# Kernel tuning notes

Hardware: AMD Instinct MI355X
Metric: run time of the kernel (lower is better)

Reference implementation:

```python
import jax, jax.numpy as jnp
import numpy as np

C = 128         # sphere_channels
H = 512         # hidden_channels
EC = 128        # edge_channels
LMAX = 4
K = 4           # num_experts
N_EQ = 2        # ceil(K/2) equivariant experts
N_NE = 2
N_NODES = 8192
N_EDGES = 262144
DEG_SIZES = np.array([2 * l + 1 for l in range(LMAX + 1)])  # [1,3,5,7,9]
M = int(DEG_SIZES.sum())  # 25 coeffs


def setup_inputs() -> dict:
    key = jax.random.key(0)
    ks = jax.random.split(key, 20)
    s = 0.02
    return {
        "x_emb": jax.random.normal(ks[0], (N_NODES, M, C), jnp.float32),
        "t_ij": jax.random.normal(ks[1], (N_EDGES, EC), jnp.float32),
        "edge_index": jax.random.randint(ks[2], (2, N_EDGES), 0, N_NODES, jnp.int32),
        # equivariant experts (stacked on leading expert axis)
        "eq_w1": jax.random.normal(ks[3], (N_EQ, C, H), jnp.float32) * s,
        "eq_gate_w": jax.random.normal(ks[4], (N_EQ, EC, H * (LMAX + 1)), jnp.float32) * s,
        "eq_gate_b": jax.random.normal(ks[5], (N_EQ, H * (LMAX + 1)), jnp.float32) * s,
        "eq_w2": jax.random.normal(ks[6], (N_EQ, H, C), jnp.float32) * s,
        # non-equivariant experts
        "ne_w1": jax.random.normal(ks[7], (N_NE, C, H), jnp.float32) * s,
        "ne_b1": jax.random.normal(ks[8], (N_NE, H), jnp.float32) * s,
        "ne_gate_w": jax.random.normal(ks[9], (N_NE, EC, H), jnp.float32) * s,
        "ne_gate_b": jax.random.normal(ks[10], (N_NE, H), jnp.float32) * s,
        "ne_w2": jax.random.normal(ks[11], (N_NE, H, C), jnp.float32) * s,
        "ne_b2": jax.random.normal(ks[12], (N_NE, C), jnp.float32) * s,
        # router
        "r_w1": jax.random.normal(ks[13], (EC, EC), jnp.float32) * s,
        "r_b1": jax.random.normal(ks[14], (EC,), jnp.float32) * s,
        "r_w2": jax.random.normal(ks[15], (EC, K), jnp.float32) * s,
        "r_b2": jax.random.normal(ks[16], (K,), jnp.float32) * s,
    }


def reference(x_emb, t_ij, edge_index, eq_w1, eq_gate_w, eq_gate_b, eq_w2,
              ne_w1, ne_b1, ne_gate_w, ne_gate_b, ne_w2, ne_b2,
              r_w1, r_b1, r_w2, r_b2):
    N = x_emb.shape[0]
    silu = jax.nn.silu

    # c_i = scatter-mean of t_ij onto destination nodes
    dst = edge_index[1]
    sums = jax.ops.segment_sum(t_ij, dst, num_segments=N)
    cnt = jax.ops.segment_sum(jnp.ones((t_ij.shape[0],), t_ij.dtype), dst, num_segments=N)
    c = sums / jnp.maximum(cnt, 1.0)[:, None]  # [N, EC]

    # soft routing weights from context
    w = jax.nn.softmax(silu(c @ r_w1 + r_b1) @ r_w2 + r_b2, axis=-1)  # [N, K]

    repeats = jnp.asarray(DEG_SIZES)
    is_scalar = (jnp.arange(M) == 0)[:, None]  # l=0 coeff mask, [M,1]

    # --- equivariant experts (vectorized over expert axis e) ---
    h = jnp.einsum('nmc,ech->enmh', x_emb, eq_w1)                      # [e,N,M,H]
    g = silu(jnp.einsum('nc,ecg->eng', c, eq_gate_w) + eq_gate_b[:, None, :])
    g = g.reshape(N_EQ, N, LMAX + 1, H)
    g = jnp.repeat(g, repeats, axis=2, total_repeat_length=M)          # [e,N,M,H]
    h = jnp.where(is_scalar, silu(h), h) * g                           # SiLU only on l=0
    out_eq = jnp.einsum('enmh,ehc->enmc', h, eq_w2)

    # --- non-equivariant experts ---
    h2 = silu(jnp.einsum('nmc,ech->enmh', x_emb, ne_w1) + ne_b1[:, None, None, :])
    g2 = silu(jnp.einsum('nc,ech->enh', c, ne_gate_w) + ne_gate_b[:, None, :])
    h2 = h2 * g2[:, :, None, :]
    out_ne = jnp.einsum('enmh,ehc->enmc', h2, ne_w2) + ne_b2[:, None, None, :]

    # softmax-weighted mixture (equiv experts first, matching ModuleList order)
    out = (jnp.einsum('nk,knmc->nmc', w[:, :N_EQ], out_eq)
           + jnp.einsum('nk,knmc->nmc', w[:, N_EQ:], out_ne))
    return out
```

## Files before the change

kernel.cpp:

```cpp
#include <hip/hip_runtime.h>

#define NNODES 8192
#define NEDGES 262144
#define CCH    128
#define HCH    512
#define GCOLS  6144
#define ROWS   204800
#define XSPAD  136
#define HGPAD  72

typedef __bf16 bf16_t;
typedef __bf16 bf16x8 __attribute__((ext_vector_type(8)));
typedef __bf16 bf16x4 __attribute__((ext_vector_type(4)));
typedef float  f32x4  __attribute__((ext_vector_type(4)));

__device__ __forceinline__ float siluf(float x) {
  return x * __builtin_amdgcn_rcpf(1.f + __expf(-x));
}

#define GLOAD_LDS(g, l) __builtin_amdgcn_global_load_lds( \
    (const __attribute__((address_space(1))) void*)(g), \
    (__attribute__((address_space(3))) void*)(l), 16, 0, 0)

constexpr size_t OFF_CSUM  = 0;
constexpr size_t OFF_DEG   = 4194304;
constexpr size_t OFF_OFFS  = 4227072;
constexpr size_t OFF_CUR   = 4263936;
constexpr size_t OFF_EIDS  = 4296704;
constexpr size_t OFF_WRT   = 5345280;
constexpr size_t OFF_CBF   = 5476352;
constexpr size_t OFF_WPT   = 7573504;
constexpr size_t OFF_BPK   = 9146368;
constexpr size_t OFF_W1T   = 9170944;
constexpr size_t OFF_W2T   = 9695232;
constexpr size_t OFF_GATES = 10219520;

__global__ __launch_bounds__(256) void edge_count_kernel(
    const int* __restrict__ edge_index, int* __restrict__ deg)
{
  int e = blockIdx.x * 256 + threadIdx.x;
  atomicAdd(&deg[edge_index[NEDGES + e]], 1);
}

__global__ __launch_bounds__(256) void scan_kernel(
    const int* __restrict__ deg, int* __restrict__ offs, int* __restrict__ cur)
{
  __shared__ int part[256];
  int t = threadIdx.x;
  int s = 0;
  #pragma unroll 4
  for (int i = 0; i < 32; ++i) s += deg[t * 32 + i];
  part[t] = s;
  __syncthreads();
  int incl = s;
  for (int off = 1; off < 256; off <<= 1) {
    int u = (t >= off) ? part[t - off] : 0;
    __syncthreads();
    incl += u;
    part[t] = incl;
    __syncthreads();
  }
  int run = incl - s;
  for (int i = 0; i < 32; ++i) {
    int d = deg[t * 32 + i];
    offs[t * 32 + i] = run;
    cur[t * 32 + i]  = run;
    run += d;
  }
  if (t == 255) offs[8192] = run;
}

__global__ __launch_bounds__(256) void edge_fill_kernel(
    const int* __restrict__ edge_index, int* __restrict__ cur, int* __restrict__ eids)
{
  int e = blockIdx.x * 256 + threadIdx.x;
  int dst = edge_index[NEDGES + e];
  int pos = atomicAdd(&cur[dst], 1);
  eids[pos] = e;
}

__global__ __launch_bounds__(128) void gather_mean_kernel(
    const float* __restrict__ t_ij, const int* __restrict__ offs,
    const int* __restrict__ eids, float* __restrict__ csum, bf16_t* __restrict__ cbf)
{
  int n = blockIdx.x, tid = threadIdx.x;
  int o0 = offs[n], o1 = offs[n + 1];
  float a0 = 0.f, a1 = 0.f;
  int j = o0;
  for (; j + 1 < o1; j += 2) {
    int e0 = eids[j], e1 = eids[j + 1];
    a0 += t_ij[(size_t)e0 * CCH + tid];
    a1 += t_ij[(size_t)e1 * CCH + tid];
  }
  if (j < o1) a0 += t_ij[(size_t)eids[j] * CCH + tid];
  float m = (a0 + a1) / fmaxf((float)(o1 - o0), 1.f);
  csum[(size_t)n * CCH + tid] = m;
  cbf[(size_t)n * CCH + tid]  = (bf16_t)m;
}

__global__ __launch_bounds__(256) void pack_kernel(
    const float* __restrict__ eq_gate_w, const float* __restrict__ ne_gate_w,
    const float* __restrict__ eq_gate_b, const float* __restrict__ ne_gate_b,
    const float* __restrict__ eq_w1, const float* __restrict__ ne_w1,
    const float* __restrict__ eq_w2, const float* __restrict__ ne_w2,
    bf16_t* __restrict__ WpackT, float* __restrict__ bpack,
    bf16_t* __restrict__ w1T, bf16_t* __restrict__ w2c)
{
  int idx = blockIdx.x * 256 + threadIdx.x;
  if (idx < 786432) {
    int j = idx >> 7, c = idx & 127;
    float v;
    if (j < 5120) { int e = j / 2560, h = j - e * 2560;
      v = eq_gate_w[(size_t)e * 327680 + (size_t)c * 2560 + h]; }
    else { int j2 = j - 5120; int e = j2 >> 9, h = j2 & 511;
      v = ne_gate_w[(size_t)e * 65536 + (size_t)c * 512 + h]; }
    WpackT[idx] = (bf16_t)v;
  } else if (idx < 792576) {
    int j = idx - 786432;
    float v;
    if (j < 5120) { int e = j / 2560; v = eq_gate_b[e * 2560 + (j - e * 2560)]; }
    else { int j2 = j - 5120; int e = j2 >> 9; v = ne_gate_b[e * 512 + (j2 & 511)]; }
    bpack[j] = v;
  } else if (idx < 1054720) {
    int i = idx - 792576;
    int e = i >> 16, rest = i & 65535, h = rest >> 7, c = rest & 127;
    float v = (e < 2) ? eq_w1[(size_t)e * 65536 + (size_t)c * 512 + h]
                      : ne_w1[(size_t)(e - 2) * 65536 + (size_t)c * 512 + h];
    w1T[i] = (bf16_t)v;
  } else if (idx < 1316864) {
    int i = idx - 1054720;
    int e = i >> 16, rest = i & 65535;
    int hc = rest >> 13, r2 = rest & 8191;
    int c = r2 >> 6, h64 = r2 & 63;
    int h = hc * 64 + h64;
    float v = (e < 2) ? eq_w2[(size_t)e * 65536 + (size_t)h * 128 + c]
                      : ne_w2[(size_t)(e - 2) * 65536 + (size_t)h * 128 + c];
    w2c[i] = (bf16_t)v;
  }
}

__global__ __launch_bounds__(128) void router_kernel(
    const float* __restrict__ c,
    const float* __restrict__ r_w1, const float* __restrict__ r_b1,
    const float* __restrict__ r_w2, const float* __restrict__ r_b2,
    float* __restrict__ wroute)
{
  __shared__ float cl[128];
  __shared__ float h1[128];
  __shared__ float lg[4];
  int n = blockIdx.x, tid = threadIdx.x;
  cl[tid] = c[(size_t)n * 128 + tid];
  __syncthreads();
  float a = 0.f;
  #pragma unroll 8
  for (int k = 0; k < 128; ++k) a += cl[k] * r_w1[k * 128 + tid];
  a += r_b1[tid];
  h1[tid] = siluf(a);
  __syncthreads();
  if (tid < 4) {
    float s = 0.f;
    for (int j = 0; j < 128; ++j) s += h1[j] * r_w2[j * 4 + tid];
    lg[tid] = s + r_b2[tid];
  }
  __syncthreads();
  if (tid == 0) {
    float m = fmaxf(fmaxf(lg[0], lg[1]), fmaxf(lg[2], lg[3]));
    float e0 = __expf(lg[0] - m), e1 = __expf(lg[1] - m);
    float e2 = __expf(lg[2] - m), e3 = __expf(lg[3] - m);
    float s = 1.f / (e0 + e1 + e2 + e3);
    f32x4 w = {e0 * s, e1 * s, e2 * s, e3 * s};
    *(f32x4*)&wroute[n * 4] = w;
  }
}

__global__ __launch_bounds__(256, 2) void gate_gemm_kernel(
    const bf16_t* __restrict__ WpackT, const bf16_t* __restrict__ cbf,
    const float* __restrict__ bpack, const float* __restrict__ wroute,
    bf16_t* __restrict__ gates, int n0)
{
  __shared__ bf16_t gt[128 * XSPAD];
  int jt = blockIdx.x, nt = blockIdx.y;
  int tid = threadIdx.x;
  int wave = tid >> 6, lane = tid & 63;
  int wr = wave >> 1, wc = wave & 1;
  int l15 = lane & 15, quad = lane >> 4;
  int ej = (jt < 20) ? 0 : (jt < 40) ? 1 : (jt < 44) ? 2 : 3;

  f32x4 acc[4][4];
  #pragma unroll
  for (int i = 0; i < 4; ++i)
    #pragma unroll
    for (int j = 0; j < 4; ++j) acc[i][j] = {0.f, 0.f, 0.f, 0.f};

  const bf16_t* abase = WpackT + ((size_t)jt * 128 + wr * 64 + l15) * 128 + quad * 8;
  const bf16_t* bbase = cbf + ((size_t)(n0 + nt * 128) + wc * 64 + l15) * 128 + quad * 8;
  float wsc[4];
  #pragma unroll
  for (int tc = 0; tc < 4; ++tc)
    wsc[tc] = wroute[(size_t)(n0 + nt * 128 + wc * 64 + tc * 16 + l15) * 4 + ej];
  #pragma unroll
  for (int ks = 0; ks < 4; ++ks) {
    bf16x8 af[4], bfr[4];
    #pragma unroll
    for (int tr = 0; tr < 4; ++tr) af[tr] = *(const bf16x8*)(abase + (size_t)tr * 16 * 128 + ks * 32);
    #pragma unroll
    for (int tc = 0; tc < 4; ++tc) bfr[tc] = *(const bf16x8*)(bbase + (size_t)tc * 16 * 128 + ks * 32);
    #pragma unroll
    for (int tr = 0; tr < 4; ++tr)
      #pragma unroll
      for (int tc = 0; tc < 4; ++tc)
        acc[tr][tc] = __builtin_amdgcn_mfma_f32_16x16x32_bf16(af[tr], bfr[tc], acc[tr][tc], 0, 0, 0);
  }
  #pragma unroll
  for (int tr = 0; tr < 4; ++tr) {
    int j0 = wr * 64 + tr * 16 + quad * 4;
    int p0 = wr * 64 + quad * 16 + tr * 4;
    f32x4 bb = *(const f32x4*)&bpack[jt * 128 + j0];
    #pragma unroll
    for (int tc = 0; tc < 4; ++tc) {
      int nl = wc * 64 + tc * 16 + l15;
      f32x4 v = acc[tr][tc];
      bf16x4 gv;
      #pragma unroll
      for (int q = 0; q < 4; ++q) gv[q] = (bf16_t)(siluf(v[q] + bb[q]) * wsc[tc]);
      *(bf16x4*)&gt[nl * XSPAD + p0] = gv;
    }
  }
  __syncthreads();
  #pragma unroll
  for (int it = 0; it < 8; ++it) {
    int idx = it * 2048 + tid * 8;
    int lr = idx >> 7, col = idx & 127;
    *(bf16x8*)&gates[((size_t)nt * 128 + lr) * GCOLS + jt * 128 + col] =
        *(const bf16x8*)&gt[lr * XSPAD + col];
  }
}

__global__ __launch_bounds__(256, 2) void fused_experts_kernel(
    const float* __restrict__ x,
    const bf16_t* __restrict__ w1T,
    const bf16_t* __restrict__ w2c,
    const bf16_t* __restrict__ gates,
    const float* __restrict__ wroute,
    const float* __restrict__ ne_b1,
    const float* __restrict__ ne_b2,
    float* __restrict__ out,
    int n0)
{
  __shared__ __align__(16) bf16_t ws1[8192];
  __shared__ __align__(16) bf16_t ws2[8192];
  __shared__ __align__(16) bf16_t hg[4 * 32 * HGPAD];

  const int tid = threadIdx.x;
  const int wave = tid >> 6, lane = tid & 63;
  const int l15 = lane & 15, quad = lane >> 4;
  const int r0 = n0 * 25 + blockIdx.x * 128;
  const int rbase = wave * 32;
  bf16_t* hgw = hg + wave * 32 * HGPAD;

  int soff1[4], soff2[4];
  #pragma unroll
  for (int i = 0; i < 4; ++i) {
    int p = wave * 4096 + i * 1024 + lane * 16;
    int row1 = p >> 8;
    soff1[i] = (row1 * 256 + ((p & 255) ^ ((row1 & 7) << 4))) >> 1;
    int row2 = p >> 7;
    soff2[i] = (row2 * 128 + ((p & 127) ^ ((row2 & 7) << 4))) >> 1;
  }
  const int swz = (l15 & 7) << 4;
  int colswz[4];
  #pragma unroll
  for (int ks = 0; ks < 4; ++ks) colswz[ks] = (ks * 64 + quad * 16) ^ swz;

  int nloc[2], lidx[2];
  f32x4 rw[2];
  bf16x8 xf[2][4];
  #pragma unroll
  for (int tc = 0; tc < 2; ++tc) {
    int r = r0 + rbase + tc * 16 + l15;
    int n = r / 25;
    int m = r - n * 25;
    nloc[tc] = n - n0;
    lidx[tc] = (m == 0) ? 0 : (m < 4) ? 1 : (m < 9) ? 2 : (m < 16) ? 3 : 4;
    rw[tc] = *(const f32x4*)&wroute[n * 4];
    const float* xr = x + (size_t)r * CCH + quad * 8;
    #pragma unroll
    for (int ks = 0; ks < 4; ++ks) {
      f32x4 a = __builtin_nontemporal_load((const f32x4*)(xr + ks * 32));
      f32x4 b = __builtin_nontemporal_load((const f32x4*)(xr + ks * 32 + 4));
      bf16x8 v;
      #pragma unroll
      for (int q = 0; q < 4; ++q) { v[q] = (bf16_t)a[q]; v[4 + q] = (bf16_t)b[q]; }
      xf[tc][ks] = v;
    }
  }

  auto gaddr = [&](int tc, int tt) -> const bf16_t* {
    int ee = tt >> 3, hh = tt & 7;
    int base = (ee < 2) ? ee * 2560 + lidx[tc] * 512 : 5120 + (ee - 2) * 512;
    return gates + (nloc[tc] * GCOLS + base + hh * 64 + quad * 16);
  };

  f32x4 oacc[8][2];
  #pragma unroll
  for (int i = 0; i < 8; ++i)
    #pragma unroll
    for (int j = 0; j < 2; ++j) oacc[i][j] = {0.f, 0.f, 0.f, 0.f};

  bf16x8 gnxa[2], gnxb[2];
  #pragma unroll
  for (int tc = 0; tc < 2; ++tc) {
    const bf16_t* gp = gaddr(tc, 0);
    gnxa[tc] = *(const bf16x8*)gp;
    gnxb[tc] = *(const bf16x8*)(gp + 8);
  }

  #pragma unroll 1
  for (int t = 0; t < 32; ++t) {
    const int e = t >> 3, hc = t & 7;
    const bool is_eq = (e < 2);

    const bf16_t* g1 = w1T + ((size_t)t << 13);
    const bf16_t* g2 = w2c + ((size_t)t << 13);
    #pragma unroll
    for (int i = 0; i < 4; ++i) {
      GLOAD_LDS(g1 + soff1[i], ws1 + wave * 2048 + i * 512);
      GLOAD_LDS(g2 + soff2[i], ws2 + wave * 2048 + i * 512);
    }
    __syncthreads();

    bf16x8 ga[2], gb[2];
    #pragma unroll
    for (int tc = 0; tc < 2; ++tc) { ga[tc] = gnxa[tc]; gb[tc] = gnxb[tc]; }
    if (t < 31) {
      #pragma unroll
      for (int tc = 0; tc < 2; ++tc) {
        const bf16_t* gp = gaddr(tc, t + 1);
        gnxa[tc] = *(const bf16x8*)gp;
        gnxb[tc] = *(const bf16x8*)(gp + 8);
      }
    }

    f32x4 hacc[4][2];
    #pragma unroll
    for (int i = 0; i < 4; ++i)
      #pragma unroll
      for (int j = 0; j < 2; ++j) hacc[i][j] = {0.f, 0.f, 0.f, 0.f};
    #pragma unroll
    for (int ks = 0; ks < 4; ++ks) {
      bf16x8 af[4];
      #pragma unroll
      for (int tr = 0; tr < 4; ++tr)
        af[tr] = *(const bf16x8*)((const char*)ws1 + (l15 + tr * 16) * 256 + colswz[ks]);
      #pragma unroll
      for (int tr = 0; tr < 4; ++tr)
        #pragma unroll
        for (int tc = 0; tc < 2; ++tc)
          hacc[tr][tc] = __builtin_amdgcn_mfma_f32_16x16x32_bf16(af[tr], xf[tc][ks], hacc[tr][tc], 0, 0, 0);
    }
    #pragma unroll
    for (int tc = 0; tc < 2; ++tc) {
      #pragma unroll
      for (int tr = 0; tr < 4; ++tr) {
        int hl = tr * 16 + quad * 4;
        f32x4 v = hacc[tr][tc];
        if (is_eq) {
          if (lidx[tc] == 0) {
            #pragma unroll
            for (int q = 0; q < 4; ++q) v[q] = siluf(v[q]);
          }
        } else {
          f32x4 b1 = *(const f32x4*)&ne_b1[(e - 2) * 512 + hc * 64 + hl];
          #pragma unroll
          for (int q = 0; q < 4; ++q) v[q] = siluf(v[q] + b1[q]);
        }
        bf16x4 hv;
        #pragma unroll
        for (int q = 0; q < 4; ++q) {
          float gf = (float)((tr < 2 ? ga[tc] : gb[tc])[(tr & 1) * 4 + q]);
          hv[q] = (bf16_t)(v[q] * gf);
        }
        *(bf16x4*)&hgw[(tc * 16 + l15) * HGPAD + hl] = hv;
      }
    }
    __builtin_amdgcn_wave_barrier();
    #pragma unroll
    for (int ks = 0; ks < 2; ++ks) {
      bf16x8 bfr[2];
      #pragma unroll
      for (int tc = 0; tc < 2; ++tc)
        bfr[tc] = *(const bf16x8*)&hgw[(tc * 16 + l15) * HGPAD + ks * 32 + quad * 8];
      #pragma unroll
      for (int tr = 0; tr < 8; ++tr) {
        bf16x8 af2 = *(const bf16x8*)((const char*)ws2 + (l15 + tr * 16) * 128 + colswz[ks]);
        #pragma unroll
        for (int tc = 0; tc < 2; ++tc)
          oacc[tr][tc] = __builtin_amdgcn_mfma_f32_16x16x32_bf16(af2, bfr[tc], oacc[tr][tc], 0, 0, 0);
      }
    }
    __syncthreads();
  }
  #pragma unroll
  for (int tc = 0; tc < 2; ++tc) {
    size_t rg = (size_t)(r0 + rbase + tc * 16 + l15);
    float wn0 = rw[tc][2], wn1 = rw[tc][3];
    #pragma unroll
    for (int tr = 0; tr < 8; ++tr) {
      int c0 = tr * 16 + quad * 4;
      f32x4 v = oacc[tr][tc];
      f32x4 b20 = *(const f32x4*)&ne_b2[c0];
      f32x4 b21 = *(const f32x4*)&ne_b2[128 + c0];
      f32x4 ov;
      #pragma unroll
      for (int q = 0; q < 4; ++q)
        ov[q] = v[q] + wn0 * b20[q] + wn1 * b21[q];
      __builtin_nontemporal_store(ov, (f32x4*)&out[rg * CCH + c0]);
    }
  }
}

extern "C" void kernel_launch(void* const* d_in, const int* in_sizes, int n_in,
                              void* d_out, int out_size, void* d_ws, size_t ws_size,
                              hipStream_t stream)
{
  const float* x_emb     = (const float*)d_in[0];
  const float* t_ij      = (const float*)d_in[1];
  const int*   edge_index= (const int*)d_in[2];
  const float* eq_w1     = (const float*)d_in[3];
  const float* eq_gate_w = (const float*)d_in[4];
  const float* eq_gate_b = (const float*)d_in[5];
  const float* eq_w2     = (const float*)d_in[6];
  const float* ne_w1     = (const float*)d_in[7];
  const float* ne_b1     = (const float*)d_in[8];
  const float* ne_gate_w = (const float*)d_in[9];
  const float* ne_gate_b = (const float*)d_in[10];
  const float* ne_w2     = (const float*)d_in[11];
  const float* ne_b2     = (const float*)d_in[12];
  const float* r_w1      = (const float*)d_in[13];
  const float* r_b1      = (const float*)d_in[14];
  const float* r_w2      = (const float*)d_in[15];
  const float* r_b2      = (const float*)d_in[16];
  float* out = (float*)d_out;

  char* ws = (char*)d_ws;
  float*  csum   = (float*)(ws + OFF_CSUM);
  int*    deg    = (int*)(ws + OFF_DEG);
  int*    offs   = (int*)(ws + OFF_OFFS);
  int*    cur    = (int*)(ws + OFF_CUR);
  int*    eids   = (int*)(ws + OFF_EIDS);
  float*  wroute = (float*)(ws + OFF_WRT);
  bf16_t* cbf    = (bf16_t*)(ws + OFF_CBF);
  bf16_t* WpackT = (bf16_t*)(ws + OFF_WPT);
  float*  bpack  = (float*)(ws + OFF_BPK);
  bf16_t* w1T    = (bf16_t*)(ws + OFF_W1T);
  bf16_t* w2c    = (bf16_t*)(ws + OFF_W2T);
  bf16_t* gates  = (bf16_t*)(ws + OFF_GATES);

  size_t avail = (ws_size > OFF_GATES) ? ws_size - OFF_GATES : 0;
  int chunk = 128;
  for (int c = NNODES; c >= 128; c >>= 1) {
    if ((size_t)c * GCOLS * sizeof(bf16_t) <= avail) { chunk = c; break; }
  }

  hipMemsetAsync(ws + OFF_DEG, 0, 32768, stream);

  edge_count_kernel<<<NEDGES / 256, 256, 0, stream>>>(edge_index, deg);
  scan_kernel<<<1, 256, 0, stream>>>(deg, offs, cur);
  edge_fill_kernel<<<NEDGES / 256, 256, 0, stream>>>(edge_index, cur, eids);
  gather_mean_kernel<<<NNODES, 128, 0, stream>>>(t_ij, offs, eids, csum, cbf);

  pack_kernel<<<5144, 256, 0, stream>>>(eq_gate_w, ne_gate_w, eq_gate_b, ne_gate_b,
                                        eq_w1, ne_w1, eq_w2, ne_w2,
                                        WpackT, bpack, w1T, w2c);
  router_kernel<<<NNODES, 128, 0, stream>>>(csum, r_w1, r_b1, r_w2, r_b2, wroute);

  for (int n0 = 0; n0 < NNODES; n0 += chunk) {
    gate_gemm_kernel<<<dim3(GCOLS / 128, chunk / 128), 256, 0, stream>>>(
        WpackT, cbf, bpack, wroute, gates, n0);
    fused_experts_kernel<<<chunk * 25 / 128, 256, 0, stream>>>(
        x_emb, w1T, w2c, gates, wroute, ne_b1, ne_b2, out, n0);
  }
}
```

Baseline: 791.1 us.

## Prefetch expert weight tiles across phases, tile pack transpose, widen gather-mean

The fused experts kernel now issues the next tile's w1 and w2 LDS loads once the current phase has finished with each buffer, so the global-to-LDS copies overlap the other phase's MFMA work instead of stalling at the top of every iteration. The wave-level barrier between the gated write and the second GEMM becomes a full block barrier, which is needed for this buffer reuse. The pack kernel uses 32x32 shared-memory tiled transposes to get coalesced reads and writes. Gather-mean uses 256 threads with float4 loads over 8 edge lanes plus a shared-memory reduction, and edge indices are read with nontemporal loads. Together these add barriers and rearrange several kernels at once.

Result: no change. 783.9 us (-0.9%).

```diff
diff --git a/kernel.cpp b/kernel.cpp
--- a/kernel.cpp
+++ b/kernel.cpp
@@ -39,7 +39,8 @@
     const int* __restrict__ edge_index, int* __restrict__ deg)
 {
   int e = blockIdx.x * 256 + threadIdx.x;
-  atomicAdd(&deg[edge_index[NEDGES + e]], 1);
+  int dst = __builtin_nontemporal_load(&edge_index[NEDGES + e]);
+  atomicAdd(&deg[dst], 1);
 }
 
 __global__ __launch_bounds__(256) void scan_kernel(
@@ -74,28 +75,44 @@
     const int* __restrict__ edge_index, int* __restrict__ cur, int* __restrict__ eids)
 {
   int e = blockIdx.x * 256 + threadIdx.x;
-  int dst = edge_index[NEDGES + e];
+  int dst = __builtin_nontemporal_load(&edge_index[NEDGES + e]);
   int pos = atomicAdd(&cur[dst], 1);
   eids[pos] = e;
 }
 
-__global__ __launch_bounds__(128) void gather_mean_kernel(
+__global__ __launch_bounds__(256) void gather_mean_kernel(
     const float* __restrict__ t_ij, const int* __restrict__ offs,
     const int* __restrict__ eids, float* __restrict__ csum, bf16_t* __restrict__ cbf)
 {
+  __shared__ float red[8][128];
   int n = blockIdx.x, tid = threadIdx.x;
+  int sub = tid & 31, rp = tid >> 5;
   int o0 = offs[n], o1 = offs[n + 1];
-  float a0 = 0.f, a1 = 0.f;
-  int j = o0;
-  for (; j + 1 < o1; j += 2) {
-    int e0 = eids[j], e1 = eids[j + 1];
-    a0 += t_ij[(size_t)e0 * CCH + tid];
-    a1 += t_ij[(size_t)e1 * CCH + tid];
-  }
-  if (j < o1) a0 += t_ij[(size_t)eids[j] * CCH + tid];
-  float m = (a0 + a1) / fmaxf((float)(o1 - o0), 1.f);
-  csum[(size_t)n * CCH + tid] = m;
-  cbf[(size_t)n * CCH + tid]  = (bf16_t)m;
+  f32x4 acc = {0.f, 0.f, 0.f, 0.f};
+  for (int j = o0 + rp; j < o1; j += 8) {
+    int e = __builtin_nontemporal_load(&eids[j]);
+    f32x4 v = __builtin_nontemporal_load((const f32x4*)&t_ij[(size_t)e * CCH + sub * 4]);
+    #pragma unroll
+    for (int q = 0; q < 4; ++q) acc[q] += v[q];
+  }
+  *(f32x4*)&red[rp][sub * 4] = acc;
+  __syncthreads();
+  if (rp == 0) {
+    float inv = 1.f / fmaxf((float)(o1 - o0), 1.f);
+    f32x4 s = {0.f, 0.f, 0.f, 0.f};
+    #pragma unroll
+    for (int k = 0; k < 8; ++k) {
+      f32x4 r = *(const f32x4*)&red[k][sub * 4];
+      #pragma unroll
+      for (int q = 0; q < 4; ++q) s[q] += r[q];
+    }
+    f32x4 m;
+    bf16x4 mb;
+    #pragma unroll
+    for (int q = 0; q < 4; ++q) { m[q] = s[q] * inv; mb[q] = (bf16_t)m[q]; }
+    *(f32x4*)&csum[(size_t)n * CCH + sub * 4] = m;
+    *(bf16x4*)&cbf[(size_t)n * CCH + sub * 4] = mb;
+  }
 }
 
 __global__ __launch_bounds__(256) void pack_kernel(
@@ -106,36 +123,59 @@
     bf16_t* __restrict__ WpackT, float* __restrict__ bpack,
     bf16_t* __restrict__ w1T, bf16_t* __restrict__ w2c)
 {
-  int idx = blockIdx.x * 256 + threadIdx.x;
-  if (idx < 786432) {
-    int j = idx >> 7, c = idx & 127;
-    float v;
-    if (j < 5120) { int e = j / 2560, h = j - e * 2560;
-      v = eq_gate_w[(size_t)e * 327680 + (size_t)c * 2560 + h]; }
-    else { int j2 = j - 5120; int e = j2 >> 9, h = j2 & 511;
-      v = ne_gate_w[(size_t)e * 65536 + (size_t)c * 512 + h]; }
-    WpackT[idx] = (bf16_t)v;
-  } else if (idx < 792576) {
-    int j = idx - 786432;
-    float v;
-    if (j < 5120) { int e = j / 2560; v = eq_gate_b[e * 2560 + (j - e * 2560)]; }
-    else { int j2 = j - 5120; int e = j2 >> 9; v = ne_gate_b[e * 512 + (j2 & 511)]; }
-    bpack[j] = v;
-  } else if (idx < 1054720) {
-    int i = idx - 792576;
-    int e = i >> 16, rest = i & 65535, h = rest >> 7, c = rest & 127;
-    float v = (e < 2) ? eq_w1[(size_t)e * 65536 + (size_t)c * 512 + h]
-                      : ne_w1[(size_t)(e - 2) * 65536 + (size_t)c * 512 + h];
-    w1T[i] = (bf16_t)v;
-  } else if (idx < 1316864) {
-    int i = idx - 1054720;
-    int e = i >> 16, rest = i & 65535;
-    int hc = rest >> 13, r2 = rest & 8191;
-    int c = r2 >> 6, h64 = r2 & 63;
-    int h = hc * 64 + h64;
-    float v = (e < 2) ? eq_w2[(size_t)e * 65536 + (size_t)h * 128 + c]
-                      : ne_w2[(size_t)(e - 2) * 65536 + (size_t)h * 128 + c];
-    w2c[i] = (bf16_t)v;
+  __shared__ float tb[32][33];
+  int b = blockIdx.x;
+  int tid = threadIdx.x, tx = tid & 31, ty = tid >> 5;
+  if (b == 1280) {
+    #pragma unroll
+    for (int it = 0; it < 24; ++it) {
+      int j = it * 256 + tid;
+      bpack[j] = (j < 5120) ? eq_gate_b[j] : ne_gate_b[j - 5120];
+    }
+    return;
+  }
+  const float* src; bf16_t* dst; int stride; bool w2mode = false;
+  int c0, h0; size_t dbase;
+  if (b < 640) {
+    int e = b / 320, r = b % 320, ct = r / 80, ht = r % 80;
+    src = eq_gate_w + (size_t)e * 327680; stride = 2560;
+    c0 = ct * 32; h0 = ht * 32;
+    dbase = ((size_t)e * 2560 + h0) * 128 + c0; dst = WpackT;
+  } else if (b < 768) {
+    int bb = b - 640, e = bb / 64, r = bb % 64, ct = r / 16, ht = r % 16;
+    src = ne_gate_w + (size_t)e * 65536; stride = 512;
+    c0 = ct * 32; h0 = ht * 32;
+    dbase = ((size_t)(5120 + e * 512) + h0) * 128 + c0; dst = WpackT;
+  } else if (b < 1024) {
+    int bb = b - 768, e = bb / 64, r = bb % 64, ct = r / 16, ht = r % 16;
+    src = (e < 2) ? eq_w1 + (size_t)e * 65536 : ne_w1 + (size_t)(e - 2) * 65536;
+    stride = 512;
+    c0 = ct * 32; h0 = ht * 32;
+    dbase = ((size_t)(e * 512) + h0) * 128 + c0; dst = w1T;
+  } else {
+    int bb = b - 1024, e = bb / 64, r = bb % 64, ht = r / 4, ct = r % 4;
+    src = (e < 2) ? eq_w2 + (size_t)e * 65536 : ne_w2 + (size_t)(e - 2) * 65536;
+    stride = 128; w2mode = true;
+    c0 = ct * 32; h0 = ht * 32;
+    dbase = (size_t)e * 65536 + (size_t)(ht >> 1) * 8192 + (size_t)c0 * 64 + (size_t)(ht & 1) * 32;
+    dst = w2c;
+  }
+  if (!w2mode) {
+    #pragma unroll
+    for (int p = 0; p < 4; ++p)
+      tb[p * 8 + ty][tx] = src[(size_t)(c0 + p * 8 + ty) * stride + h0 + tx];
+    __syncthreads();
+    #pragma unroll
+    for (int p = 0; p < 4; ++p)
+      dst[dbase + (size_t)(p * 8 + ty) * 128 + tx] = (bf16_t)tb[tx][p * 8 + ty];
+  } else {
+    #pragma unroll
+    for (int p = 0; p < 4; ++p)
+      tb[p * 8 + ty][tx] = src[(size_t)(h0 + p * 8 + ty) * 128 + c0 + tx];
+    __syncthreads();
+    #pragma unroll
+    for (int p = 0; p < 4; ++p)
+      dst[dbase + (size_t)(p * 8 + ty) * 64 + tx] = (bf16_t)tb[tx][p * 8 + ty];
   }
 }
 
@@ -314,20 +354,17 @@
     gnxa[tc] = *(const bf16x8*)gp;
     gnxb[tc] = *(const bf16x8*)(gp + 8);
   }
+  #pragma unroll
+  for (int i = 0; i < 4; ++i) {
+    GLOAD_LDS(w1T + soff1[i], ws1 + wave * 2048 + i * 512);
+    GLOAD_LDS(w2c + soff2[i], ws2 + wave * 2048 + i * 512);
+  }
+  __syncthreads();
 
   #pragma unroll 1
   for (int t = 0; t < 32; ++t) {
     const int e = t >> 3, hc = t & 7;
     const bool is_eq = (e < 2);
-
-    const bf16_t* g1 = w1T + ((size_t)t << 13);
-    const bf16_t* g2 = w2c + ((size_t)t << 13);
-    #pragma unroll
-    for (int i = 0; i < 4; ++i) {
-      GLOAD_LDS(g1 + soff1[i], ws1 + wave * 2048 + i * 512);
-      GLOAD_LDS(g2 + soff2[i], ws2 + wave * 2048 + i * 512);
-    }
-    __syncthreads();
 
     bf16x8 ga[2], gb[2];
     #pragma unroll
@@ -383,7 +420,13 @@
         *(bf16x4*)&hgw[(tc * 16 + l15) * HGPAD + hl] = hv;
       }
     }
-    __builtin_amdgcn_wave_barrier();
+    __syncthreads();
+    if (t < 31) {
+      const bf16_t* g1 = w1T + ((size_t)(t + 1) << 13);
+      #pragma unroll
+      for (int i = 0; i < 4; ++i)
+        GLOAD_LDS(g1 + soff1[i], ws1 + wave * 2048 + i * 512);
+    }
     #pragma unroll
     for (int ks = 0; ks < 2; ++ks) {
       bf16x8 bfr[2];
@@ -399,6 +442,12 @@
       }
     }
     __syncthreads();
+    if (t < 31) {
+      const bf16_t* g2 = w2c + ((size_t)(t + 1) << 13);
+      #pragma unroll
+      for (int i = 0; i < 4; ++i)
+        GLOAD_LDS(g2 + soff2[i], ws2 + wave * 2048 + i * 512);
+    }
   }
   #pragma unroll
   for (int tc = 0; tc < 2; ++tc) {
@@ -467,9 +516,9 @@
   edge_count_kernel<<<NEDGES / 256, 256, 0, stream>>>(edge_index, deg);
   scan_kernel<<<1, 256, 0, stream>>>(deg, offs, cur);
   edge_fill_kernel<<<NEDGES / 256, 256, 0, stream>>>(edge_index, cur, eids);
-  gather_mean_kernel<<<NNODES, 128, 0, stream>>>(t_ij, offs, eids, csum, cbf);
-
-  pack_kernel<<<5144, 256, 0, stream>>>(eq_gate_w, ne_gate_w, eq_gate_b, ne_gate_b,
+  gather_mean_kernel<<<NNODES, 256, 0, stream>>>(t_ij, offs, eids, csum, cbf);
+
+  pack_kernel<<<1281, 256, 0, stream>>>(eq_gate_w, ne_gate_w, eq_gate_b, ne_gate_b,
                                         eq_w1, ne_w1, eq_w2, ne_w2,
                                         WpackT, bpack, w1T, w2c);
   router_kernel<<<NNODES, 128, 0, stream>>>(csum, r_w1, r_b1, r_w2, r_b2, wroute);
```
